# Performance work log

Hardware: AMD Instinct MI355X
Metric: run time of the kernel (lower is better)

Reference implementation:

```python
import jax, jax.numpy as jnp
import numpy as np
from jax import lax

B = 32
ITERS = 100
ALPHA = 0.3  # keras LeakyReLU default alpha
BN_SCALE = np.float32(1.0 / np.sqrt(1.0 + 1e-3))  # inference BN, default moving stats (mean 0, var 1)


def _make_psf_mat():
    # Gaussian PSF mapping 5184 fine (72x72) code positions -> 81 coarse (9x9) pixels, mat shape (5184, 81)
    sigma = (150.0 / 100.0) * 9.0 / 64.0
    coarse = np.arange(9) + 0.5
    fine = (np.arange(72) + 0.5) * 9.0 / 72.0
    g = np.exp(-(fine[:, None] - coarse[None, :]) ** 2 / (2.0 * sigma ** 2))  # (72, 9)
    mat = np.einsum('ia,jb->ijab', g, g).reshape(5184, 81)
    mat = mat / np.linalg.norm(mat, ord=2)  # spectral-normalize so FISTA (mu=1) is stable
    return mat.astype(np.float32)


def leaky(x):
    return jnp.where(x >= 0, x, ALPHA * x)


def conv(x, k, strides=(1, 1)):
    return lax.conv_general_dilated(x, k, strides, 'SAME',
                                    dimension_numbers=('NHWC', 'HWIO', 'NHWC'))


def _forward(inp, mat, w1_k, w1_b, x1_k, x1_b, c51_k, c51_b, c15_k, c15_b,
             c55_k, c55_b, x2_k, x2_b, y17_k, y17_b, y71_k, y71_b, yc_k, yc_b,
             d1_k, d2_k, h1_w, h1_b, h2_w, h2_b, h3_w, h3_b):
    b = inp.shape[0]
    # w branch
    w = leaky(conv(inp, w1_k) + w1_b)  # (B,9,9,1)
    # z branch -> lambda parameter
    z = inp * BN_SCALE
    z = leaky(conv(z, d1_k, strides=(3, 3)) * BN_SCALE)  # (B,3,3,12), downsample: conv no-bias + BN + LeakyReLU
    z = leaky(conv(z, d2_k, strides=(3, 3)) * BN_SCALE)  # (B,1,1,24)
    z = z.reshape(b, -1)
    z = z @ h1_w + h1_b
    z = z @ h2_w + h2_b
    z = z @ h3_w + h3_b  # (B,1)
    param = 0.1 * jax.nn.sigmoid(z)  # (B,1)
    # x branch: normalize (max of |x| over axis 1 only, as in source)
    x = inp / (0.001 + jnp.max(jnp.abs(inp), axis=1, keepdims=True))
    x = leaky(conv(x, x1_k) + x1_b)  # (B,9,9,3)
    # --- CompressedSensing: 100-iter FISTA, vectorized over batch and 3 channels ---
    im = x.reshape(b, 81, 3).transpose(0, 2, 1)  # (B,3,81) row-major flatten per channel
    lam = (param * 0.1)[:, :, None]  # (B,1,1), mu = 1.0

    def step(carry, _):
        y_tmp, y_last, t = carry
        resid = im - jnp.einsum('bcn,nk->bck', y_tmp, mat)      # (B,3,81)  = im - mat^T y
        re = jnp.einsum('bck,nk->bcn', resid, mat)              # (B,3,5184) = mat (im - mat^T y)
        wv = y_tmp + re
        y_new = jax.nn.relu(wv - lam) - jax.nn.relu(-wv - lam)  # soft threshold
        t_n = (1.0 + jnp.sqrt(1.0 + 4.0 * t * t)) / 2.0
        y_next = y_new + (t - 1.0) / t_n * (y_new - y_last)
        return (y_next, y_new, t_n), None

    init = (jnp.zeros((b, 3, 5184), jnp.float32),
            jnp.zeros((b, 3, 5184), jnp.float32),
            jnp.float32(1.0))
    (_, y_new, _), _ = lax.scan(step, init, None, length=ITERS)
    cs_out = y_new.transpose(0, 2, 1).reshape(b, 72, 72, 3)  # stack channels last then reshape
    x = conv(cs_out, c51_k, strides=(2, 2)) + c51_b   # (B,36,36,16), no activation
    x = conv(x, c15_k, strides=(2, 2)) + c15_b        # (B,18,18,32)
    x = conv(x, c55_k, strides=(2, 2)) + c55_b        # (B,9,9,64)
    x = leaky(conv(x, x2_k) + x2_b)                   # (B,9,9,8)
    # y branch
    y1 = conv(inp, y17_k) + y17_b                     # (B,9,9,32)
    y2 = conv(inp, y71_k) + y71_b                     # (B,9,9,32)
    y = leaky(conv(jnp.concatenate([y1, y2], axis=-1), yc_k) + yc_b)  # (B,9,9,32)
    out = jnp.concatenate([w, x, y], axis=-1)         # (B,9,9,41)
    return out, cs_out


def setup_inputs() -> dict:
    key = jax.random.key(0)
    ks = jax.random.split(key, 20)
    rn = lambda k, s, sc=0.1: sc * jax.random.normal(k, s, dtype=jnp.float32)
    x1_k = jnp.clip(1.0 + 0.3 * jax.random.normal(ks[1], (1, 1, 3, 3)), 0.0, None).astype(jnp.float32)
    return {
        'inp': jax.random.normal(ks[0], (B, 9, 9, 3), dtype=jnp.float32),
        'mat': jnp.asarray(_make_psf_mat()),
        'w1_k': rn(ks[2], (1, 1, 3, 1)), 'w1_b': jnp.zeros((1,), jnp.float32),
        'x1_k': x1_k, 'x1_b': jnp.zeros((3,), jnp.float32),
        'c51_k': rn(ks[3], (5, 1, 3, 16)), 'c51_b': jnp.zeros((16,), jnp.float32),
        'c15_k': rn(ks[4], (1, 5, 16, 32)), 'c15_b': jnp.zeros((32,), jnp.float32),
        'c55_k': rn(ks[5], (5, 5, 32, 64)), 'c55_b': jnp.zeros((64,), jnp.float32),
        'x2_k': rn(ks[6], (1, 1, 64, 8)), 'x2_b': jnp.zeros((8,), jnp.float32),
        'y17_k': rn(ks[7], (1, 7, 3, 32)), 'y17_b': jnp.zeros((32,), jnp.float32),
        'y71_k': rn(ks[8], (7, 1, 3, 32)), 'y71_b': jnp.zeros((32,), jnp.float32),
        'yc_k': rn(ks[9], (1, 1, 64, 32)), 'yc_b': jnp.zeros((32,), jnp.float32),
        'd1_k': rn(ks[10], (5, 5, 3, 12)), 'd2_k': rn(ks[11], (5, 5, 12, 24)),
        'h1_w': rn(ks[12], (24, 24), 0.2), 'h1_b': jnp.zeros((24,), jnp.float32),
        'h2_w': rn(ks[13], (24, 12), 0.2), 'h2_b': jnp.zeros((12,), jnp.float32),
        'h3_w': rn(ks[14], (12, 1), 0.2), 'h3_b': jnp.zeros((1,), jnp.float32),
    }


def reference(inp, mat, w1_k, w1_b, x1_k, x1_b, c51_k, c51_b, c15_k, c15_b,
              c55_k, c55_b, x2_k, x2_b, y17_k, y17_b, y71_k, y71_b, yc_k, yc_b,
              d1_k, d2_k, h1_w, h1_b, h2_w, h2_b, h3_w, h3_b):
    return _forward(inp, mat, w1_k, w1_b, x1_k, x1_b, c51_k, c51_b, c15_k, c15_b,
                    c55_k, c55_b, x2_k, x2_b, y17_k, y17_b, y71_k, y71_b, yc_k, yc_b,
                    d1_k, d2_k, h1_w, h1_b, h2_w, h2_b, h3_w, h3_b)
```

## Files before the change

kernel.cpp:

```cpp
#include <hip/hip_runtime.h>
#include <math.h>

#define LEAKY(x) ((x) >= 0.f ? (x) : 0.3f*(x))

#define G_OFF   0
#define IM_OFF  648
#define LAM_OFF 8424
#define WB_OFF  8456
#define YBR_OFF 11048
#define X1_OFF  93992
#define X2_OFF  757544
#define X3_OFF  1089320

#define OUT0 106272

__global__ __launch_bounds__(256) void prep_kernel(
    const float* __restrict__ inp, const float* __restrict__ mat,
    const float* __restrict__ w1_k, const float* __restrict__ w1_b,
    const float* __restrict__ x1_k, const float* __restrict__ x1_b,
    const float* __restrict__ y17_k, const float* __restrict__ y17_b,
    const float* __restrict__ y71_k, const float* __restrict__ y71_b,
    const float* __restrict__ yc_k, const float* __restrict__ yc_b,
    const float* __restrict__ d1_k, const float* __restrict__ d2_k,
    const float* __restrict__ h1_w, const float* __restrict__ h1_b,
    const float* __restrict__ h2_w, const float* __restrict__ h2_b,
    const float* __restrict__ h3_w, const float* __restrict__ h3_b,
    float* __restrict__ ws)
{
    int t = threadIdx.x;
    if (blockIdx.x == 0) {
        float rs = rsqrtf(mat[0]);
        for (int u = t; u < 648; u += 256) {
            int i = u / 9, a = u % 9;
            ws[G_OFF + u] = mat[(size_t)(i*72)*81 + a*9] * rs;
        }
        return;
    }
    int b = blockIdx.x - 1;
    __shared__ float sin_[243];
    __shared__ float cm[27];
    __shared__ float cat[5184];
    __shared__ float z1[108];
    __shared__ float z2[24];
    __shared__ float v1[24];
    __shared__ float v2[12];

    const float BN  = 1.0f / sqrtf(1.001f);
    const float BN2 = BN * BN;

    for (int u = t; u < 243; u += 256) sin_[u] = inp[b*243 + u];
    __syncthreads();

    if (t < 81) {
        float s = w1_b[0];
        for (int i = 0; i < 3; ++i) s += sin_[t*3+i] * w1_k[i];
        ws[WB_OFF + b*81 + t] = LEAKY(s);
    } else if (t < 108) {
        int u = t - 81;
        float m = 0.f;
        for (int r = 0; r < 9; ++r) m = fmaxf(m, fabsf(sin_[r*27 + u]));
        cm[u] = 0.001f + m;
    }
    if (t >= 128 && t < 236) {
        int u = t - 128;
        int o = u % 12, ox = (u/12) % 3, oy = u/36;
        float s = 0.f;
        for (int kh = 0; kh < 5; ++kh) {
            int iy = oy*3 - 1 + kh;
            if (iy < 0 || iy > 8) continue;
            for (int kw = 0; kw < 5; ++kw) {
                int ix = ox*3 - 1 + kw;
                if (ix < 0 || ix > 8) continue;
                for (int i = 0; i < 3; ++i)
                    s += sin_[(iy*9+ix)*3 + i] * d1_k[((kh*5+kw)*3 + i)*12 + o];
            }
        }
        z1[u] = LEAKY(BN2 * s);
    }
    __syncthreads();

    if (t < 243) {
        int o = t / 81, p = t % 81;
        int c = p % 9;
        float s = x1_b[o];
        for (int i = 0; i < 3; ++i)
            s += (sin_[p*3+i] / cm[c*3+i]) * x1_k[i*3 + o];
        ws[IM_OFF + (b*3 + o)*81 + p] = LEAKY(s);
    }
    __syncthreads();

    if (t < 24) {
        float s = 0.f;
        for (int kh = 1; kh < 4; ++kh)
            for (int kw = 1; kw < 4; ++kw)
                for (int i = 0; i < 12; ++i)
                    s += z1[((kh-1)*3 + (kw-1))*12 + i] * d2_k[((kh*5+kw)*12 + i)*24 + t];
        z2[t] = LEAKY(BN * s);
    }
    __syncthreads();
    if (t < 24) {
        float s = h1_b[t];
        for (int i = 0; i < 24; ++i) s += z2[i] * h1_w[i*24 + t];
        v1[t] = s;
    }
    __syncthreads();
    if (t < 12) {
        float s = h2_b[t];
        for (int i = 0; i < 24; ++i) s += v1[i] * h2_w[i*12 + t];
        v2[t] = s;
    }
    __syncthreads();
    if (t == 0) {
        float s = h3_b[0];
        for (int i = 0; i < 12; ++i) s += v2[i] * h3_w[i];
        ws[LAM_OFF + b] = 0.01f / (1.f + expf(-s));
    }

    for (int u = t; u < 5184; u += 256) {
        int pos = u / 64, i = u % 64;
        int r = pos / 9, c = pos % 9;
        float s;
        if (i < 32) {
            s = y17_b[i];
            for (int kw = 0; kw < 7; ++kw) {
                int cc = c - 3 + kw;
                if (cc < 0 || cc > 8) continue;
                for (int ii = 0; ii < 3; ++ii)
                    s += sin_[(r*9+cc)*3 + ii] * y17_k[(kw*3+ii)*32 + i];
            }
        } else {
            int i2 = i - 32;
            s = y71_b[i2];
            for (int kh = 0; kh < 7; ++kh) {
                int rr = r - 3 + kh;
                if (rr < 0 || rr > 8) continue;
                for (int ii = 0; ii < 3; ++ii)
                    s += sin_[(rr*9+c)*3 + ii] * y71_k[(kh*3+ii)*32 + i2];
            }
        }
        cat[pos*64 + i] = s;
    }
    __syncthreads();
    for (int u = t; u < 2592; u += 256) {
        int pos = u / 32, o = u % 32;
        float s = yc_b[o];
        for (int i = 0; i < 64; ++i) s += cat[pos*64 + i] * yc_k[i*32 + o];
        ws[YBR_OFF + (b*81 + pos)*32 + o] = LEAKY(s);
    }
}

__global__ __launch_bounds__(512, 2) void fista_kernel(
    const float* __restrict__ ws, float* __restrict__ cs_out)
{
    __shared__ __align__(16) float Qt[648];
    __shared__ __align__(16) float U[9*432];
    __shared__ __align__(16) float T[9*76];
    __shared__ __align__(16) float P[6*84];
    __shared__ __align__(16) float R[108];

    int t = threadIdx.x;
    int b = blockIdx.x / 3, ch = blockIdx.x % 3;
    const float* g = ws + G_OFF;
    float lam = ws[LAM_OFF + b];

    int j = t % 72, grp = t / 72;
    bool act = t < 432;

    float Gr[108];
    if (act) {
#pragma unroll
        for (int s = 0; s < 12; ++s)
#pragma unroll
            for (int a = 0; a < 9; ++a)
                Gr[s*9 + a] = g[(grp*12 + s)*9 + a];
    }
    float Gj[9];
    if (act) {
#pragma unroll
        for (int a = 0; a < 9; ++a) Gj[a] = g[j*9 + a];
    }
    int pa = t / 54, prem = t % 54, pb = prem / 6, pseg = prem % 6;
    float GTr[12];
    if (t < 486) {
#pragma unroll
        for (int r = 0; r < 12; ++r) GTr[r] = g[(pseg*12 + r)*9 + pb];
    }
    float im_ab = 0.f;
    if (t < 81) im_ab = ws[IM_OFF + (b*3 + ch)*81 + t];
    if (t < 108) {
        int a = t / 12, c = t % 12;
        R[t] = (c < 9) ? ws[IM_OFF + (b*3 + ch)*81 + a*9 + c] : 0.f;
    }

    float Yv[12], Yl[12];
#pragma unroll
    for (int s = 0; s < 12; ++s) { Yv[s] = 0.f; Yl[s] = 0.f; }
    float tk = 1.f;
    __syncthreads();

    for (int it = 0; it < 100; ++it) {
        if (act) {
            const float4* R4 = (const float4*)(R + grp*12);
            float4 r0 = R4[0], r1 = R4[1], r2 = R4[2];
            Qt[grp*72 + j] =
                r0.x*Gj[0] + r0.y*Gj[1] + r0.z*Gj[2] + r0.w*Gj[3]
              + r1.x*Gj[4] + r1.y*Gj[5] + r1.z*Gj[6] + r1.w*Gj[7]
              + r2.x*Gj[8];
        }
        if (t < 216) {
            int a2 = 6 + t/72;
            const float4* R4 = (const float4*)(R + a2*12);
            float4 r0 = R4[0], r1 = R4[1], r2 = R4[2];
            Qt[a2*72 + j] =
                r0.x*Gj[0] + r0.y*Gj[1] + r0.z*Gj[2] + r0.w*Gj[3]
              + r1.x*Gj[4] + r1.y*Gj[5] + r1.z*Gj[6] + r1.w*Gj[7]
              + r2.x*Gj[8];
        }
        __syncthreads();
        float tn = 0.5f*(1.f + sqrtf(1.f + 4.f*tk*tk));
        float cmom = (tk - 1.f) / tn;
        tk = tn;
        if (act) {
            float q0 = Qt[0*72+j], q1 = Qt[1*72+j], q2 = Qt[2*72+j],
                  q3 = Qt[3*72+j], q4 = Qt[4*72+j], q5 = Qt[5*72+j],
                  q6 = Qt[6*72+j], q7 = Qt[7*72+j], q8 = Qt[8*72+j];
            float u0=0,u1=0,u2=0,u3=0,u4=0,u5=0,u6=0,u7=0,u8=0;
#pragma unroll
            for (int s = 0; s < 12; ++s) {
                float re = Gr[s*9+0]*q0 + Gr[s*9+1]*q1 + Gr[s*9+2]*q2
                         + Gr[s*9+3]*q3 + Gr[s*9+4]*q4 + Gr[s*9+5]*q5
                         + Gr[s*9+6]*q6 + Gr[s*9+7]*q7 + Gr[s*9+8]*q8;
                float wv = Yv[s] + re;
                float aa = fabsf(wv) - lam;
                float yn = aa > 0.f ? copysignf(aa, wv) : 0.f;
                float yx = yn + cmom*(yn - Yl[s]);
                Yl[s] = yn; Yv[s] = yx;
                u0 += yx*Gr[s*9+0]; u1 += yx*Gr[s*9+1]; u2 += yx*Gr[s*9+2];
                u3 += yx*Gr[s*9+3]; u4 += yx*Gr[s*9+4]; u5 += yx*Gr[s*9+5];
                u6 += yx*Gr[s*9+6]; u7 += yx*Gr[s*9+7]; u8 += yx*Gr[s*9+8];
            }
            U[0*432+t]=u0; U[1*432+t]=u1; U[2*432+t]=u2; U[3*432+t]=u3;
            U[4*432+t]=u4; U[5*432+t]=u5; U[6*432+t]=u6; U[7*432+t]=u7;
            U[8*432+t]=u8;
        }
        if (it == 99) break;
        __syncthreads();
        if (act) {
            float s = U[grp*432 + j]       + U[grp*432 + 72 + j]
                    + U[grp*432 + 144 + j] + U[grp*432 + 216 + j]
                    + U[grp*432 + 288 + j] + U[grp*432 + 360 + j];
            T[grp*76 + j] = s;
        }
        if (t < 216) {
            int a2 = 6 + t/72;
            float s = U[a2*432 + j]       + U[a2*432 + 72 + j]
                    + U[a2*432 + 144 + j] + U[a2*432 + 216 + j]
                    + U[a2*432 + 288 + j] + U[a2*432 + 360 + j];
            T[a2*76 + j] = s;
        }
        __syncthreads();
        if (t < 486) {
            const float4* T4 = (const float4*)(T + pa*76 + pseg*12);
            float4 t0 = T4[0], t1 = T4[1], t2 = T4[2];
            P[pseg*84 + pa*9 + pb] =
                t0.x*GTr[0] + t0.y*GTr[1] + t0.z*GTr[2] + t0.w*GTr[3]
              + t1.x*GTr[4] + t1.y*GTr[5] + t1.z*GTr[6] + t1.w*GTr[7]
              + t2.x*GTr[8] + t2.y*GTr[9] + t2.z*GTr[10]+ t2.w*GTr[11];
        }
        __syncthreads();
        if (t < 81) {
            float s = P[t] + P[84+t] + P[168+t] + P[252+t] + P[336+t] + P[420+t];
            R[(t/9)*12 + (t%9)] = im_ab - s;
        }
        __syncthreads();
    }
    if (act) {
#pragma unroll
        for (int s = 0; s < 12; ++s) {
            int i = grp*12 + s;
            cs_out[(size_t)(b*5184 + i*72 + j)*3 + ch] = Yl[s];
        }
    }
}

__global__ __launch_bounds__(256) void c51_kernel(
    const float* __restrict__ cs, const float* __restrict__ k,
    const float* __restrict__ bias, float* __restrict__ out)
{
    int id = blockIdx.x*256 + threadIdx.x;
    if (id >= 32*36*36*16) return;
    int o = id & 15; int rest = id >> 4;
    int ox = rest % 36; rest /= 36; int oy = rest % 36; int b = rest / 36;
    float s = bias[o];
    int ix = ox*2;
    for (int kh = 0; kh < 5; ++kh) {
        int iy = oy*2 - 1 + kh;
        if (iy < 0 || iy >= 72) continue;
        const float* p = cs + ((size_t)(b*72 + iy)*72 + ix)*3;
        const float* kk = k + kh*48 + o;
        s += p[0]*kk[0] + p[1]*kk[16] + p[2]*kk[32];
    }
    out[id] = s;
}

__global__ __launch_bounds__(256) void c15_kernel(
    const float* __restrict__ x1, const float* __restrict__ k,
    const float* __restrict__ bias, float* __restrict__ out)
{
    int id = blockIdx.x*256 + threadIdx.x;
    if (id >= 32*18*18*32) return;
    int o = id & 31; int rest = id >> 5;
    int ox = rest % 18; rest /= 18; int oy = rest % 18; int b = rest / 18;
    float s = bias[o];
    int iy = oy*2;
    for (int kw = 0; kw < 5; ++kw) {
        int ix = ox*2 - 1 + kw;
        if (ix < 0 || ix >= 36) continue;
        const float* p = x1 + ((size_t)(b*36 + iy)*36 + ix)*16;
        const float* kk = k + kw*512 + o;
        for (int i = 0; i < 16; ++i) s += p[i]*kk[i*32];
    }
    out[id] = s;
}

__global__ __launch_bounds__(256) void c55_kernel(
    const float* __restrict__ x2, const float* __restrict__ k,
    const float* __restrict__ bias, float* __restrict__ out)
{
    int id = blockIdx.x*256 + threadIdx.x;
    if (id >= 32*9*9*64) return;
    int o = id & 63; int rest = id >> 6;
    int ox = rest % 9; rest /= 9; int oy = rest % 9; int b = rest / 9;
    float s = bias[o];
    for (int kh = 0; kh < 5; ++kh) {
        int iy = oy*2 - 1 + kh;
        if (iy < 0 || iy >= 18) continue;
        for (int kw = 0; kw < 5; ++kw) {
            int ix = ox*2 - 1 + kw;
            if (ix < 0 || ix >= 18) continue;
            const float* p = x2 + ((size_t)(b*18 + iy)*18 + ix)*32;
            const float* kk = k + (kh*5+kw)*2048 + o;
            for (int i = 0; i < 32; ++i) s += p[i]*kk[i*64];
        }
    }
    out[id] = s;
}

__global__ __launch_bounds__(256) void out_kernel(
    const float* __restrict__ ws, const float* __restrict__ x2_k,
    const float* __restrict__ x2_b, float* __restrict__ out)
{
    int id = blockIdx.x*256 + threadIdx.x;
    if (id >= OUT0) return;
    int q = id % 41; int rest = id / 41;
    int cc = rest % 9; rest /= 9; int r = rest % 9; int b = rest / 9;
    float val;
    if (q == 0) {
        val = ws[WB_OFF + b*81 + r*9 + cc];
    } else if (q <= 8) {
        int o = q - 1;
        const float* p = ws + X3_OFF + ((size_t)(b*9 + r)*9 + cc)*64;
        float s = x2_b[o];
        for (int i = 0; i < 64; ++i) s += p[i]*x2_k[i*8 + o];
        val = LEAKY(s);
    } else {
        val = ws[YBR_OFF + ((size_t)(b*81 + r*9 + cc))*32 + (q - 9)];
    }
    out[id] = val;
}

extern "C" void kernel_launch(void* const* d_in, const int* in_sizes, int n_in,
                              void* d_out, int out_size, void* d_ws, size_t ws_size,
                              hipStream_t stream) {
    const float* inp   = (const float*)d_in[0];
    const float* mat   = (const float*)d_in[1];
    const float* w1_k  = (const float*)d_in[2];
    const float* w1_b  = (const float*)d_in[3];
    const float* x1_k  = (const float*)d_in[4];
    const float* x1_b  = (const float*)d_in[5];
    const float* c51_k = (const float*)d_in[6];
    const float* c51_b = (const float*)d_in[7];
    const float* c15_k = (const float*)d_in[8];
    const float* c15_b = (const float*)d_in[9];
    const float* c55_k = (const float*)d_in[10];
    const float* c55_b = (const float*)d_in[11];
    const float* x2_k  = (const float*)d_in[12];
    const float* x2_b  = (const float*)d_in[13];
    const float* y17_k = (const float*)d_in[14];
    const float* y17_b = (const float*)d_in[15];
    const float* y71_k = (const float*)d_in[16];
    const float* y71_b = (const float*)d_in[17];
    const float* yc_k  = (const float*)d_in[18];
    const float* yc_b  = (const float*)d_in[19];
    const float* d1_k  = (const float*)d_in[20];
    const float* d2_k  = (const float*)d_in[21];
    const float* h1_w  = (const float*)d_in[22];
    const float* h1_b  = (const float*)d_in[23];
    const float* h2_w  = (const float*)d_in[24];
    const float* h2_b  = (const float*)d_in[25];
    const float* h3_w  = (const float*)d_in[26];
    const float* h3_b  = (const float*)d_in[27];

    float* ws  = (float*)d_ws;
    float* out = (float*)d_out;
    float* cs  = out + OUT0;

    hipLaunchKernelGGL(prep_kernel, dim3(33), dim3(256), 0, stream,
        inp, mat, w1_k, w1_b, x1_k, x1_b, y17_k, y17_b, y71_k, y71_b,
        yc_k, yc_b, d1_k, d2_k, h1_w, h1_b, h2_w, h2_b, h3_w, h3_b, ws);
    hipLaunchKernelGGL(fista_kernel, dim3(96), dim3(512), 0, stream, ws, cs);
    hipLaunchKernelGGL(c51_kernel, dim3(2592), dim3(256), 0, stream, cs, c51_k, c51_b, ws + X1_OFF);
    hipLaunchKernelGGL(c15_kernel, dim3(1296), dim3(256), 0, stream, ws + X1_OFF, c15_k, c15_b, ws + X2_OFF);
    hipLaunchKernelGGL(c55_kernel, dim3(648), dim3(256), 0, stream, ws + X2_OFF, c55_k, c55_b, ws + X3_OFF);
    hipLaunchKernelGGL(out_kernel, dim3(416), dim3(256), 0, stream, ws, x2_k, x2_b, out);
}
```

Baseline: 399.5 us.

## Replace FISTA shared-memory reductions with LDS atomics and fuse c55 with output assembly

Each FISTA iteration now accumulates the partial U sums and the P projections straight into T and R with shared-memory atomicAdd. This drops two staging buffers and two __syncthreads per iteration. Idle threads (t>=432) reset R to the image and zero T, so that work overlaps with the main compute. The c55 convolution is fused with the 1x1 x2 conv and final output packing into one kernel that holds weights in registers, which removes the X3 round trip and one launch. In exchange, atomics make float summation order nondeterministic and add LDS contention, and the fused kernel launches only 288 small blocks.

```diff
diff --git a/kernel.cpp b/kernel.cpp
--- a/kernel.cpp
+++ b/kernel.cpp
@@ -10,7 +10,6 @@
 #define YBR_OFF 11048
 #define X1_OFF  93992
 #define X2_OFF  757544
-#define X3_OFF  1089320
 
 #define OUT0 106272
 
@@ -152,11 +151,9 @@
 __global__ __launch_bounds__(512, 2) void fista_kernel(
     const float* __restrict__ ws, float* __restrict__ cs_out)
 {
-    __shared__ __align__(16) float Qt[648];
-    __shared__ __align__(16) float U[9*432];
-    __shared__ __align__(16) float T[9*76];
-    __shared__ __align__(16) float P[6*84];
-    __shared__ __align__(16) float R[108];
+    __shared__ float Qt[648];
+    __shared__ float T[684];
+    __shared__ float R[108];
 
     int t = threadIdx.x;
     int b = blockIdx.x / 3, ch = blockIdx.x % 3;
@@ -185,8 +182,12 @@
 #pragma unroll
         for (int r = 0; r < 12; ++r) GTr[r] = g[(pseg*12 + r)*9 + pb];
     }
-    float im_ab = 0.f;
-    if (t < 81) im_ab = ws[IM_OFF + (b*3 + ch)*81 + t];
+    float imA = 0.f, imB = 0.f;
+    if (t >= 432) {
+        int e = t - 432;
+        imA = ws[IM_OFF + (b*3 + ch)*81 + e];
+        if (e == 0) imB = ws[IM_OFF + (b*3 + ch)*81 + 80];
+    }
     if (t < 108) {
         int a = t / 12, c = t % 12;
         R[t] = (c < 9) ? ws[IM_OFF + (b*3 + ch)*81 + a*9 + c] : 0.f;
@@ -206,6 +207,9 @@
                 r0.x*Gj[0] + r0.y*Gj[1] + r0.z*Gj[2] + r0.w*Gj[3]
               + r1.x*Gj[4] + r1.y*Gj[5] + r1.z*Gj[6] + r1.w*Gj[7]
               + r2.x*Gj[8];
+        } else {
+            for (int u = t - 432; u < 648; u += 80)
+                T[(u/72)*76 + (u%72)] = 0.f;
         }
         if (t < 216) {
             int a2 = 6 + t/72;
@@ -239,38 +243,28 @@
                 u3 += yx*Gr[s*9+3]; u4 += yx*Gr[s*9+4]; u5 += yx*Gr[s*9+5];
                 u6 += yx*Gr[s*9+6]; u7 += yx*Gr[s*9+7]; u8 += yx*Gr[s*9+8];
             }
-            U[0*432+t]=u0; U[1*432+t]=u1; U[2*432+t]=u2; U[3*432+t]=u3;
-            U[4*432+t]=u4; U[5*432+t]=u5; U[6*432+t]=u6; U[7*432+t]=u7;
-            U[8*432+t]=u8;
+            if (it < 99) {
+                atomicAdd(&T[0*76+j], u0); atomicAdd(&T[1*76+j], u1);
+                atomicAdd(&T[2*76+j], u2); atomicAdd(&T[3*76+j], u3);
+                atomicAdd(&T[4*76+j], u4); atomicAdd(&T[5*76+j], u5);
+                atomicAdd(&T[6*76+j], u6); atomicAdd(&T[7*76+j], u7);
+                atomicAdd(&T[8*76+j], u8);
+            }
+        } else {
+            int e = t - 432;
+            R[(e/9)*12 + (e%9)] = imA;
+            if (e == 0) R[8*12 + 8] = imB;
         }
         if (it == 99) break;
-        __syncthreads();
-        if (act) {
-            float s = U[grp*432 + j]       + U[grp*432 + 72 + j]
-                    + U[grp*432 + 144 + j] + U[grp*432 + 216 + j]
-                    + U[grp*432 + 288 + j] + U[grp*432 + 360 + j];
-            T[grp*76 + j] = s;
-        }
-        if (t < 216) {
-            int a2 = 6 + t/72;
-            float s = U[a2*432 + j]       + U[a2*432 + 72 + j]
-                    + U[a2*432 + 144 + j] + U[a2*432 + 216 + j]
-                    + U[a2*432 + 288 + j] + U[a2*432 + 360 + j];
-            T[a2*76 + j] = s;
-        }
         __syncthreads();
         if (t < 486) {
             const float4* T4 = (const float4*)(T + pa*76 + pseg*12);
             float4 t0 = T4[0], t1 = T4[1], t2 = T4[2];
-            P[pseg*84 + pa*9 + pb] =
+            float s =
                 t0.x*GTr[0] + t0.y*GTr[1] + t0.z*GTr[2] + t0.w*GTr[3]
               + t1.x*GTr[4] + t1.y*GTr[5] + t1.z*GTr[6] + t1.w*GTr[7]
               + t2.x*GTr[8] + t2.y*GTr[9] + t2.z*GTr[10]+ t2.w*GTr[11];
-        }
-        __syncthreads();
-        if (t < 81) {
-            float s = P[t] + P[84+t] + P[168+t] + P[252+t] + P[336+t] + P[420+t];
-            R[(t/9)*12 + (t%9)] = im_ab - s;
+            atomicAdd(&R[pa*12 + pb], -s);
         }
         __syncthreads();
     }
@@ -323,50 +317,62 @@
     out[id] = s;
 }
 
-__global__ __launch_bounds__(256) void c55_kernel(
+__global__ __launch_bounds__(128) void c55out_kernel(
     const float* __restrict__ x2, const float* __restrict__ k,
-    const float* __restrict__ bias, float* __restrict__ out)
+    const float* __restrict__ bias, const float* __restrict__ ws,
+    const float* __restrict__ x2_k, const float* __restrict__ x2_b,
+    float* __restrict__ out)
 {
-    int id = blockIdx.x*256 + threadIdx.x;
-    if (id >= 32*9*9*64) return;
-    int o = id & 63; int rest = id >> 6;
-    int ox = rest % 9; rest /= 9; int oy = rest % 9; int b = rest / 9;
-    float s = bias[o];
+    __shared__ float sx3[9*65];
+    int t = threadIdx.x;
+    int b = blockIdx.x / 9, oy = blockIdx.x % 9;
+    int o = t & 63;
+    int w = t >> 6;
+    int ox0 = w ? 5 : 0;
+    int nox = w ? 4 : 5;
+
+    float acc[5];
+#pragma unroll
+    for (int q = 0; q < 5; ++q) acc[q] = bias[o];
+
     for (int kh = 0; kh < 5; ++kh) {
         int iy = oy*2 - 1 + kh;
         if (iy < 0 || iy >= 18) continue;
         for (int kw = 0; kw < 5; ++kw) {
-            int ix = ox*2 - 1 + kw;
-            if (ix < 0 || ix >= 18) continue;
-            const float* p = x2 + ((size_t)(b*18 + iy)*18 + ix)*32;
-            const float* kk = k + (kh*5+kw)*2048 + o;
-            for (int i = 0; i < 32; ++i) s += p[i]*kk[i*64];
-        }
-    }
-    out[id] = s;
-}
-
-__global__ __launch_bounds__(256) void out_kernel(
-    const float* __restrict__ ws, const float* __restrict__ x2_k,
-    const float* __restrict__ x2_b, float* __restrict__ out)
-{
-    int id = blockIdx.x*256 + threadIdx.x;
-    if (id >= OUT0) return;
-    int q = id % 41; int rest = id / 41;
-    int cc = rest % 9; rest /= 9; int r = rest % 9; int b = rest / 9;
-    float val;
-    if (q == 0) {
-        val = ws[WB_OFF + b*81 + r*9 + cc];
-    } else if (q <= 8) {
-        int o = q - 1;
-        const float* p = ws + X3_OFF + ((size_t)(b*9 + r)*9 + cc)*64;
-        float s = x2_b[o];
-        for (int i = 0; i < 64; ++i) s += p[i]*x2_k[i*8 + o];
-        val = LEAKY(s);
-    } else {
-        val = ws[YBR_OFF + ((size_t)(b*81 + r*9 + cc))*32 + (q - 9)];
-    }
-    out[id] = val;
+            const float* kk = k + ((size_t)(kh*5 + kw)*32)*64 + o;
+            float kv[32];
+#pragma unroll
+            for (int i = 0; i < 32; ++i) kv[i] = kk[i*64];
+            for (int q = 0; q < nox; ++q) {
+                int ix = (ox0 + q)*2 - 1 + kw;
+                if (ix < 0 || ix >= 18) continue;
+                const float4* p4 = (const float4*)(x2 + ((size_t)(b*18 + iy)*18 + ix)*32);
+#pragma unroll
+                for (int m = 0; m < 8; ++m) {
+                    float4 pv = p4[m];
+                    acc[q] += pv.x*kv[m*4] + pv.y*kv[m*4+1]
+                            + pv.z*kv[m*4+2] + pv.w*kv[m*4+3];
+                }
+            }
+        }
+    }
+    for (int q = 0; q < nox; ++q) sx3[(ox0 + q)*65 + o] = acc[q];
+    __syncthreads();
+
+    if (t < 72) {
+        int cc = t / 8, q = t % 8;
+        float s = x2_b[q];
+        for (int i = 0; i < 64; ++i) s += sx3[cc*65 + i] * x2_k[i*8 + q];
+        out[((size_t)(b*9 + oy)*9 + cc)*41 + 1 + q] = LEAKY(s);
+    }
+    for (int e = t; e < 297; e += 128) {
+        int cc = e / 33, kq = e % 33;
+        float val;
+        int q;
+        if (kq == 0) { val = ws[WB_OFF + b*81 + oy*9 + cc]; q = 0; }
+        else { val = ws[YBR_OFF + ((size_t)(b*81 + oy*9 + cc))*32 + (kq - 1)]; q = kq + 8; }
+        out[((size_t)(b*9 + oy)*9 + cc)*41 + q] = val;
+    }
 }
 
 extern "C" void kernel_launch(void* const* d_in, const int* in_sizes, int n_in,
@@ -411,6 +417,6 @@
     hipLaunchKernelGGL(fista_kernel, dim3(96), dim3(512), 0, stream, ws, cs);
     hipLaunchKernelGGL(c51_kernel, dim3(2592), dim3(256), 0, stream, cs, c51_k, c51_b, ws + X1_OFF);
     hipLaunchKernelGGL(c15_kernel, dim3(1296), dim3(256), 0, stream, ws + X1_OFF, c15_k, c15_b, ws + X2_OFF);
-    hipLaunchKernelGGL(c55_kernel, dim3(648), dim3(256), 0, stream, ws + X2_OFF, c55_k, c55_b, ws + X3_OFF);
-    hipLaunchKernelGGL(out_kernel, dim3(416), dim3(256), 0, stream, ws, x2_k, x2_b, out);
-}
+    hipLaunchKernelGGL(c55out_kernel, dim3(288), dim3(128), 0, stream,
+        ws + X2_OFF, c55_k, c55_b, ws, x2_k, x2_b, out);
+}
```

Result: slower. 971.1 us (+143.1%).
